# Performance work log

Hardware: AMD Instinct MI355X
Metric: run time of the kernel (lower is better)

The kernel has to match this reference:

```python
import jax, jax.numpy as jnp
import numpy as np

NUM_HEADS = 16


def _rope_tables(seq_len, head_dim, dtype):
    # angles[n, j] = n * 10000^(-2j/head_dim)
    pos = jnp.arange(seq_len, dtype=jnp.float32)
    inv = jnp.power(10000.0, -2.0 * jnp.arange(head_dim // 2, dtype=jnp.float32) / head_dim)
    ang = pos[:, None] * inv[None, :]                     # [N, D/2]
    # repeat_interleave(.., 2): [c0,c0,c1,c1,...]
    cos = jnp.repeat(jnp.cos(ang), 2, axis=-1).astype(dtype)  # [N, D]
    sin = jnp.repeat(jnp.sin(ang), 2, axis=-1).astype(dtype)  # [N, D]
    return cos[None, None], sin[None, None]               # [1,1,N,D]


def _rotate_half_interleaved(x):
    # stack([-x[...,1::2], x[...,::2]], -1).reshape_as(x)
    x2 = jnp.stack([-x[..., 1::2], x[..., ::2]], axis=-1)
    return x2.reshape(x.shape)


def setup_inputs() -> dict:
    key = jax.random.key(0)
    k0, k1, k2, k3 = jax.random.split(key, 4)
    B, N, C = 2, 2048, 1024
    s = 1.0 / np.sqrt(C)
    return {
        "x": jax.random.normal(k0, (B, N, C), dtype=jnp.float32),
        "Wq": jax.random.normal(k1, (C, C), dtype=jnp.float32) * s,
        "Wk": jax.random.normal(k2, (C, C), dtype=jnp.float32) * s,
        "Wv": jax.random.normal(k3, (C, C), dtype=jnp.float32) * s,
    }


def reference(x, Wq, Wk, Wv):
    B, N, C = x.shape
    H = NUM_HEADS
    D = C // H
    scale = D ** -0.5

    def heads(y):  # [B,N,C] -> [B,H,N,D]
        return y.reshape(B, N, H, D).transpose(0, 2, 1, 3)

    # nn.Linear: y = x @ W.T
    q = heads(x @ Wq.T)
    k = heads(x @ Wk.T)
    v = heads(x @ Wv.T)

    cos, sin = _rope_tables(N, D, x.dtype)
    q = q * cos + _rotate_half_interleaved(q) * sin
    k = k * cos + _rotate_half_interleaved(k) * sin

    attn = jnp.einsum("bhnd,bhmd->bhnm", q, k) * scale
    attn = jax.nn.softmax(attn, axis=-1)          # dropout p=0.0 -> identity
    out = jnp.einsum("bhnm,bhmd->bhnd", attn, v)
    return out.transpose(0, 2, 1, 3).reshape(B, N, C)
```

## Files before the change

### kernel.cpp

```cpp
#include <hip/hip_runtime.h>

typedef _Float16 f16;
typedef _Float16 f16x2 __attribute__((ext_vector_type(2)));
typedef _Float16 f16x8 __attribute__((ext_vector_type(8)));
typedef _Float16 f16x4 __attribute__((ext_vector_type(4)));
typedef float f32x4 __attribute__((ext_vector_type(4)));

#define GAS(p) ((const __attribute__((address_space(1))) void*)(p))
#define LAS(p) ((__attribute__((address_space(3))) void*)(p))

__device__ __forceinline__ f32x4 mfma16(f16x8 a, f16x8 b, f32x4 c) {
  return __builtin_amdgcn_mfma_f32_16x16x32_f16(a, b, c, 0, 0, 0);
}

__device__ __forceinline__ f16x2 cvt2(float a, float b) {
  return __builtin_bit_cast(f16x2, __builtin_amdgcn_cvt_pkrtz(a, b));
}

__device__ __forceinline__ void stage_tile(const f16* __restrict__ grow0,
                                           int stride_f16, f16* lds, int t) {
  int r = t >> 3;
  int sw = ((t & 7) ^ (r & 7)) * 8;
  __builtin_amdgcn_global_load_lds(GAS(grow0 + r * stride_f16 + sw),
                                   LAS(lds + t * 8), 16, 0, 0);
}

__global__ void convall(const float* __restrict__ x, const float* __restrict__ wq,
                        const float* __restrict__ wk, const float* __restrict__ wv,
                        f16* __restrict__ xh, f16* __restrict__ wh,
                        float* __restrict__ cosT, float* __restrict__ sinT) {
  int bid = blockIdx.x;
  if (bid >= 3584) {
    int idx = (bid - 3584) * 256 + threadIdx.x;
    int n = idx >> 5, jj = idx & 31;
    float inv = powf(10000.0f, -(float)jj * (1.0f / 32.0f));
    float ang = (float)n * inv;
    cosT[idx] = cosf(ang);
    sinT[idx] = sinf(ang);
    return;
  }
  const float* s;
  f16* d;
  int boff;
  if (bid < 2048)      { s = x;  d = xh;            boff = bid; }
  else if (bid < 2560) { s = wq; d = wh;            boff = bid - 2048; }
  else if (bid < 3072) { s = wk; d = wh + 1048576;  boff = bid - 2560; }
  else                 { s = wv; d = wh + 2097152;  boff = bid - 3072; }
  int i = (boff * 256 + threadIdx.x) * 8;
  float4 a = *(const float4*)(s + i);
  float4 b = *(const float4*)(s + i + 4);
  f16x8 o = {(f16)a.x, (f16)a.y, (f16)a.z, (f16)a.w,
             (f16)b.x, (f16)b.y, (f16)b.z, (f16)b.w};
  *(f16x8*)(d + i) = o;
}

__global__ __launch_bounds__(256, 3) void qkv_gemm(
    const f16* __restrict__ X, const f16* __restrict__ W,
    const float* __restrict__ cosT, const float* __restrict__ sinT,
    f16* __restrict__ Q, f16* __restrict__ K, f16* __restrict__ Vt) {
  __shared__ f16 As[128 * 64];
  __shared__ f16 Bs[128 * 64];
  const int tid = threadIdx.x;
  const int wv = tid >> 6, lane = tid & 63;
  const int m0 = blockIdx.x * 128, n0 = blockIdx.y * 128;
  const int cl = lane & 15, g = lane >> 4;
  const int wr = (wv >> 1) * 64, wc = (wv & 1) * 64;
  const int vx = cl & 7;

  f32x4 acc[4][4] = {};
  const f16* ga = X + (size_t)m0 * 1024;
  const f16* gb = W + (size_t)n0 * 1024;

  for (int kt = 0; kt < 1024; kt += 64) {
    __syncthreads();
#pragma unroll
    for (int rd = 0; rd < 4; ++rd) {
      stage_tile(ga + kt, 1024, As, tid + rd * 256);
      stage_tile(gb + kt, 1024, Bs, tid + rd * 256);
    }
    __syncthreads();
#pragma unroll
    for (int kk = 0; kk < 2; ++kk) {
      f16x8 a[4], bf[4];
#pragma unroll
      for (int mi = 0; mi < 4; ++mi)
        a[mi] = *(const f16x8*)(As + (wr + mi * 16 + cl) * 64 +
                                (((kk * 4 + g) ^ vx) << 3));
#pragma unroll
      for (int ni = 0; ni < 4; ++ni)
        bf[ni] = *(const f16x8*)(Bs + (wc + ni * 16 + cl) * 64 +
                                 (((kk * 4 + g) ^ vx) << 3));
#pragma unroll
      for (int mi = 0; mi < 4; ++mi)
#pragma unroll
        for (int ni = 0; ni < 4; ++ni)
          acc[mi][ni] = mfma16(a[mi], bf[ni], acc[mi][ni]);
    }
  }

  const int p = n0 >> 10;
  for (int mi = 0; mi < 4; ++mi) {
    int rbase = m0 + wr + mi * 16 + g * 4;
    for (int ni = 0; ni < 4; ++ni) {
      int gc = n0 + wc + ni * 16 + cl;
      int f = gc & 1023;
      int h = f >> 6, d = f & 63;
      if (p < 2) {
        int j = d >> 1;
        f16* dst = (p == 0) ? Q : K;
        float sc = (p == 0) ? 0.18033688011f : 1.0f;
        for (int r = 0; r < 4; ++r) {
          int row = rbase + r;
          int bb = row >> 11, n = row & 2047;
          float co = cosT[n * 32 + j], si = sinT[n * 32 + j];
          float v = acc[mi][ni][r];
          float pr = __shfl_xor(v, 1);
          float o = (d & 1) ? (v * co + pr * si) : (v * co - pr * si);
          dst[((bb * 16 + h) * 2048 + n) * 64 + d] = (f16)(o * sc);
        }
      } else {
        int bb = rbase >> 11, n = rbase & 2047;
        int np = (n & ~31) | (((n >> 2) & 3) << 3) | (((n >> 4) & 1) << 2);
        f16x4 pk = {(f16)acc[mi][ni][0], (f16)acc[mi][ni][1],
                    (f16)acc[mi][ni][2], (f16)acc[mi][ni][3]};
        *(f16x4*)(Vt + (size_t)((bb * 16 + h) * 64 + d) * 2048 + np) = pk;
      }
    }
  }
}

__global__ __launch_bounds__(256, 2) void attn(
    const f16* __restrict__ Q, const f16* __restrict__ K,
    const f16* __restrict__ Vt, float* __restrict__ out) {
  __shared__ f16 Ks[2][2][4096];
  __shared__ f16 Vs[2][2][4096];
  const int tid = threadIdx.x;
  const int w = tid >> 6, lane = tid & 63;
  const int cl = lane & 15, g = lane >> 4;
  const int id = blockIdx.x;
  const int xcd = id & 7, j = id >> 3;
  const int bh = xcd * 4 + (j >> 4);
  const int b = bh >> 4, h = bh & 15;
  const int qb = (j & 15) * 128 + w * 32;
  const f16* Qp = Q + (size_t)bh * (2048 * 64);
  const f16* Kp = K + (size_t)bh * (2048 * 64);
  const f16* Vp = Vt + (size_t)bh * (64 * 2048);

  f16x8 bq[2][2];
#pragma unroll
  for (int qh = 0; qh < 2; ++qh) {
    bq[qh][0] = *(const f16x8*)(Qp + (qb + qh * 16 + cl) * 64 + g * 8);
    bq[qh][1] = *(const f16x8*)(Qp + (qb + qh * 16 + cl) * 64 + 32 + g * 8);
  }

  f32x4 acc[2][4] = {};
  float lsp[2] = {0.f, 0.f};
  const int vx = cl & 7;
  const f32x4 z4 = {0.f, 0.f, 0.f, 0.f};
  union PB { f16x8 v; f16x2 hx[4]; };

  auto STAGE = [&](int it, int bf) {
    const f16* kp = Kp + (size_t)it * 8192;
    const f16* vp = Vp + (size_t)it * 128;
#pragma unroll
    for (int hh = 0; hh < 2; ++hh) {
      stage_tile(kp + hh * 4096, 64, Ks[bf][hh], tid);
      stage_tile(kp + hh * 4096, 64, Ks[bf][hh], tid + 256);
      stage_tile(vp + hh * 64, 2048, Vs[bf][hh], tid);
      stage_tile(vp + hh * 64, 2048, Vs[bf][hh], tid + 256);
    }
  };

  auto BODY = [&](const f16* kb, const f16* vb) {
    f16x8 a0[4], a1[4];
#pragma unroll
    for (int i = 0; i < 4; ++i) {
      const f16* kr = kb + (i * 16 + cl) * 64;
      a0[i] = *(const f16x8*)(kr + ((g ^ vx) << 3));
      a1[i] = *(const f16x8*)(kr + (((4 + g) ^ vx) << 3));
    }
    f32x4 s[2][4];
    __builtin_amdgcn_s_setprio(1);
#pragma unroll
    for (int qh = 0; qh < 2; ++qh)
#pragma unroll
      for (int i = 0; i < 4; ++i)
        s[qh][i] = mfma16(a1[i], bq[qh][1], mfma16(a0[i], bq[qh][0], z4));
    __builtin_amdgcn_s_setprio(0);
    PB pb[2][2];
#pragma unroll
    for (int qh = 0; qh < 2; ++qh) {
      float p0 = exp2f(s[qh][0][0]), p1 = exp2f(s[qh][0][1]);
      float p2 = exp2f(s[qh][0][2]), p3 = exp2f(s[qh][0][3]);
      float p4 = exp2f(s[qh][1][0]), p5 = exp2f(s[qh][1][1]);
      float p6 = exp2f(s[qh][1][2]), p7 = exp2f(s[qh][1][3]);
      float p8 = exp2f(s[qh][2][0]), p9 = exp2f(s[qh][2][1]);
      float pa = exp2f(s[qh][2][2]), pc = exp2f(s[qh][2][3]);
      float pd = exp2f(s[qh][3][0]), pe = exp2f(s[qh][3][1]);
      float pf = exp2f(s[qh][3][2]), pg = exp2f(s[qh][3][3]);
      lsp[qh] += (((p0 + p1) + (p2 + p3)) + ((p4 + p5) + (p6 + p7))) +
                 (((p8 + p9) + (pa + pc)) + ((pd + pe) + (pf + pg)));
      pb[qh][0].hx[0] = cvt2(p0, p1); pb[qh][0].hx[1] = cvt2(p2, p3);
      pb[qh][0].hx[2] = cvt2(p4, p5); pb[qh][0].hx[3] = cvt2(p6, p7);
      pb[qh][1].hx[0] = cvt2(p8, p9); pb[qh][1].hx[1] = cvt2(pa, pc);
      pb[qh][1].hx[2] = cvt2(pd, pe); pb[qh][1].hx[3] = cvt2(pf, pg);
    }
    __builtin_amdgcn_s_setprio(1);
#pragma unroll
    for (int ks = 0; ks < 2; ++ks) {
#pragma unroll
      for (int d = 0; d < 4; ++d) {
        const f16* vr = vb + (d * 16 + cl) * 64;
        f16x8 va = *(const f16x8*)(vr + (((ks * 4 + g) ^ vx) << 3));
        acc[0][d] = mfma16(va, pb[0][ks].v, acc[0][d]);
        acc[1][d] = mfma16(va, pb[1][ks].v, acc[1][d]);
      }
    }
    __builtin_amdgcn_s_setprio(0);
  };

  STAGE(0, 0);
  int cur = 0;
  for (int it = 0; it < 16; ++it) {
    asm volatile("s_waitcnt vmcnt(0)" ::: "memory");
    __builtin_amdgcn_s_barrier();
    if (it + 1 < 16) STAGE(it + 1, cur ^ 1);
    BODY(Ks[cur][0], Vs[cur][0]);
    BODY(Ks[cur][1], Vs[cur][1]);
    cur ^= 1;
  }

#pragma unroll
  for (int qh = 0; qh < 2; ++qh) {
    float ls = lsp[qh];
    ls += __shfl_xor(ls, 16);
    ls += __shfl_xor(ls, 32);
    float inv = 1.0f / ls;
    float* ob = out + (size_t)(b * 2048 + qb + qh * 16 + cl) * 1024 +
                h * 64 + g * 4;
#pragma unroll
    for (int d = 0; d < 4; ++d) {
      float4 o = {acc[qh][d][0] * inv, acc[qh][d][1] * inv,
                  acc[qh][d][2] * inv, acc[qh][d][3] * inv};
      *(float4*)(ob + (size_t)d * 16) = o;
    }
  }
}

extern "C" void kernel_launch(void* const* d_in, const int* in_sizes, int n_in,
                              void* d_out, int out_size, void* d_ws, size_t ws_size,
                              hipStream_t stream) {
  const float* x  = (const float*)d_in[0];
  const float* Wq = (const float*)d_in[1];
  const float* Wk = (const float*)d_in[2];
  const float* Wv = (const float*)d_in[3];
  float* out = (float*)d_out;
  char* ws = (char*)d_ws;

  f16* xh   = (f16*)(ws);
  f16* wh   = (f16*)(ws + 8388608);
  f16* Qr   = (f16*)(ws + 14680064);
  f16* Kr   = (f16*)(ws + 23068672);
  f16* Vt   = (f16*)(ws + 31457280);
  float* cosT = (float*)(ws + 39845888);
  float* sinT = (float*)(ws + 40108032);

  convall<<<3840, 256, 0, stream>>>(x, Wq, Wk, Wv, xh, wh, cosT, sinT);

  dim3 g1(32, 24);
  qkv_gemm<<<g1, 256, 0, stream>>>(xh, wh, cosT, sinT, Qr, Kr, Vt);

  attn<<<512, 256, 0, stream>>>(Qr, Kr, Vt, out);
}
```

Measured before the change: 97.72 us.

## Software-pipeline QK^T MFMA of next half-tile against softmax and PV

Splits the attention body into a QK-score phase, which also preloads V fragments from LDS, and a softmax plus PV phase. The loop is reordered so the next half-tile's score MFMAs are issued before the current half-tile's exp/convert/PV work. The aim is to overlap MFMA latency with the transcendental work and to hide LDS read latency. It also restructures the double-buffer barrier schedule. In exchange it keeps two sets of score and V-fragment registers live at once, which raises VGPR pressure and may lower occupancy.

```diff
diff --git a/kernel.cpp b/kernel.cpp
--- a/kernel.cpp
+++ b/kernel.cpp
@@ -158,6 +158,7 @@
   const int vx = cl & 7;
   const f32x4 z4 = {0.f, 0.f, 0.f, 0.f};
   union PB { f16x8 v; f16x2 hx[4]; };
+  struct AS { f32x4 s[2][4]; f16x8 vf[2][4]; };
 
   auto STAGE = [&](int it, int bf) {
     const f16* kp = Kp + (size_t)it * 8192;
@@ -171,7 +172,7 @@
     }
   };
 
-  auto BODY = [&](const f16* kb, const f16* vb) {
+  auto APH = [&](const f16* kb, const f16* vb, AS& S) {
     f16x8 a0[4], a1[4];
 #pragma unroll
     for (int i = 0; i < 4; ++i) {
@@ -179,25 +180,33 @@
       a0[i] = *(const f16x8*)(kr + ((g ^ vx) << 3));
       a1[i] = *(const f16x8*)(kr + (((4 + g) ^ vx) << 3));
     }
-    f32x4 s[2][4];
+#pragma unroll
+    for (int ks = 0; ks < 2; ++ks)
+#pragma unroll
+      for (int d = 0; d < 4; ++d)
+        S.vf[ks][d] = *(const f16x8*)(vb + (d * 16 + cl) * 64 +
+                                      (((ks * 4 + g) ^ vx) << 3));
     __builtin_amdgcn_s_setprio(1);
 #pragma unroll
     for (int qh = 0; qh < 2; ++qh)
 #pragma unroll
       for (int i = 0; i < 4; ++i)
-        s[qh][i] = mfma16(a1[i], bq[qh][1], mfma16(a0[i], bq[qh][0], z4));
+        S.s[qh][i] = mfma16(a1[i], bq[qh][1], mfma16(a0[i], bq[qh][0], z4));
     __builtin_amdgcn_s_setprio(0);
+  };
+
+  auto BPH = [&](AS& S) {
     PB pb[2][2];
 #pragma unroll
     for (int qh = 0; qh < 2; ++qh) {
-      float p0 = exp2f(s[qh][0][0]), p1 = exp2f(s[qh][0][1]);
-      float p2 = exp2f(s[qh][0][2]), p3 = exp2f(s[qh][0][3]);
-      float p4 = exp2f(s[qh][1][0]), p5 = exp2f(s[qh][1][1]);
-      float p6 = exp2f(s[qh][1][2]), p7 = exp2f(s[qh][1][3]);
-      float p8 = exp2f(s[qh][2][0]), p9 = exp2f(s[qh][2][1]);
-      float pa = exp2f(s[qh][2][2]), pc = exp2f(s[qh][2][3]);
-      float pd = exp2f(s[qh][3][0]), pe = exp2f(s[qh][3][1]);
-      float pf = exp2f(s[qh][3][2]), pg = exp2f(s[qh][3][3]);
+      float p0 = exp2f(S.s[qh][0][0]), p1 = exp2f(S.s[qh][0][1]);
+      float p2 = exp2f(S.s[qh][0][2]), p3 = exp2f(S.s[qh][0][3]);
+      float p4 = exp2f(S.s[qh][1][0]), p5 = exp2f(S.s[qh][1][1]);
+      float p6 = exp2f(S.s[qh][1][2]), p7 = exp2f(S.s[qh][1][3]);
+      float p8 = exp2f(S.s[qh][2][0]), p9 = exp2f(S.s[qh][2][1]);
+      float pa = exp2f(S.s[qh][2][2]), pc = exp2f(S.s[qh][2][3]);
+      float pd = exp2f(S.s[qh][3][0]), pe = exp2f(S.s[qh][3][1]);
+      float pf = exp2f(S.s[qh][3][2]), pg = exp2f(S.s[qh][3][3]);
       lsp[qh] += (((p0 + p1) + (p2 + p3)) + ((p4 + p5) + (p6 + p7))) +
                  (((p8 + p9) + (pa + pc)) + ((pd + pe) + (pf + pg)));
       pb[qh][0].hx[0] = cvt2(p0, p1); pb[qh][0].hx[1] = cvt2(p2, p3);
@@ -207,27 +216,35 @@
     }
     __builtin_amdgcn_s_setprio(1);
 #pragma unroll
-    for (int ks = 0; ks < 2; ++ks) {
+    for (int ks = 0; ks < 2; ++ks)
 #pragma unroll
       for (int d = 0; d < 4; ++d) {
-        const f16* vr = vb + (d * 16 + cl) * 64;
-        f16x8 va = *(const f16x8*)(vr + (((ks * 4 + g) ^ vx) << 3));
-        acc[0][d] = mfma16(va, pb[0][ks].v, acc[0][d]);
-        acc[1][d] = mfma16(va, pb[1][ks].v, acc[1][d]);
+        acc[0][d] = mfma16(S.vf[ks][d], pb[0][ks].v, acc[0][d]);
+        acc[1][d] = mfma16(S.vf[ks][d], pb[1][ks].v, acc[1][d]);
       }
-    }
     __builtin_amdgcn_s_setprio(0);
   };
 
   STAGE(0, 0);
-  int cur = 0;
+  asm volatile("s_waitcnt vmcnt(0)" ::: "memory");
+  __builtin_amdgcn_s_barrier();
+  STAGE(1, 1);
+  AS P, Qs;
+  APH(Ks[0][0], Vs[0][0], P);
+
   for (int it = 0; it < 16; ++it) {
-    asm volatile("s_waitcnt vmcnt(0)" ::: "memory");
-    __builtin_amdgcn_s_barrier();
-    if (it + 1 < 16) STAGE(it + 1, cur ^ 1);
-    BODY(Ks[cur][0], Vs[cur][0]);
-    BODY(Ks[cur][1], Vs[cur][1]);
-    cur ^= 1;
+    const int c = it & 1;
+    APH(Ks[c][1], Vs[c][1], Qs);
+    BPH(P);
+    if (it < 15) {
+      asm volatile("s_waitcnt vmcnt(0)" ::: "memory");
+      __builtin_amdgcn_s_barrier();
+      if (it + 2 < 16) STAGE(it + 2, c);
+      APH(Ks[c ^ 1][0], Vs[c ^ 1][0], P);
+      BPH(Qs);
+    } else {
+      BPH(Qs);
+    }
   }
 
 #pragma unroll
```

Result: no change. 97.23 us (-0.5%).
